# Kernel optimization log

Hardware: AMD Instinct MI355X
Metric: run time of the kernel (lower is better)

## Reference

```python
import jax, jax.numpy as jnp
import numpy as np

B, N_IN, N_VALUES = 1_000_000, 59, 12


def setup_inputs() -> dict:
    key = jax.random.key(0)
    k1, k2, k3, k4 = jax.random.split(key, 4)
    neural_activity = jax.random.normal(k1, (B, N_IN), dtype=jnp.float32)
    cards_by_trials = jax.random.randint(k2, (B, 4, 3), 0, N_VALUES, dtype=jnp.int64)
    # nn.Linear params: weight [out, in], bias [out]
    W = jax.random.normal(k3, (N_VALUES, N_IN), dtype=jnp.float32) / np.sqrt(N_IN)
    b = jax.random.normal(k4, (N_VALUES,), dtype=jnp.float32) * 0.01
    return {"neural_activity": neural_activity, "cards_by_trials": cards_by_trials, "W": W, "b": b}


def reference(neural_activity, cards_by_trials, W, b):
    # feature_values: [B, n_values]
    feature_values = jnp.einsum("bi,vi->bv", neural_activity, W) + b
    # fused gather + per-card sum (replaces the Python double loop)
    batch_idx = jnp.arange(feature_values.shape[0])[:, None, None]  # [B,1,1]
    gathered = feature_values[batch_idx, cards_by_trials]           # [B,4,3]
    card_values = jnp.sum(gathered, axis=-1)                        # [B,4]
    return card_values
```

## Files before the change

kernel.cpp:

```cpp
#include <hip/hip_runtime.h>

#define N_IN 59
#define N_VALUES 12
#define BLOCK 256
#define WROWS 16
#define TILE_F (WROWS * N_IN)
#define TILE_BYTES (TILE_F * 4)
#define TILE_STRIDE_F 952
#define FV_STRIDE 12
#define WL_STRIDE 68
#define WL_FLOATS (16 * WL_STRIDE)
#define GRID 3125
#define WAVES 4
#define TOTWAVES (GRID * WAVES)
#define TPW 5

typedef __attribute__((ext_vector_type(4))) float  f32x4;
typedef __attribute__((ext_vector_type(8))) __bf16 bf16x8;

#define STAGE(tt)                                                              \
    do {                                                                       \
        const char* _s = (const char*)act + (long)(tt) * TILE_BYTES + lane * 16;\
        char* _d = (char*)tw;                                                  \
        __builtin_amdgcn_global_load_lds(                                      \
            (const __attribute__((address_space(1))) void*)(_s),               \
            (__attribute__((address_space(3))) void*)(_d), 16, 0, 0);          \
        __builtin_amdgcn_global_load_lds(                                      \
            (const __attribute__((address_space(1))) void*)(_s + 1024),        \
            (__attribute__((address_space(3))) void*)(_d + 1024), 16, 0, 0);   \
        __builtin_amdgcn_global_load_lds(                                      \
            (const __attribute__((address_space(1))) void*)(_s + 2048),        \
            (__attribute__((address_space(3))) void*)(_d + 2048), 16, 0, 0);   \
        if (lane < 44) {                                                       \
            __builtin_amdgcn_global_load_lds(                                  \
                (const __attribute__((address_space(1))) void*)(_s + 3072),    \
                (__attribute__((address_space(3))) void*)(_d + 3072), 16, 0, 0);\
        }                                                                      \
    } while (0)

__global__ __launch_bounds__(BLOCK, 8) void value_model_kernel(
    const float* __restrict__ act,
    const int*   __restrict__ cards,
    const float* __restrict__ W,
    const float* __restrict__ bias,
    float* __restrict__ out)
{
    __shared__ float aLds[WAVES * TILE_STRIDE_F];
    __shared__ float xLds[WL_FLOATS];

    const int tid  = threadIdx.x;
    const int wave = tid >> 6;
    const int lane = tid & 63;
    float* tw = aLds + wave * TILE_STRIDE_F;

    for (int i = tid; i < WL_FLOATS; i += BLOCK) xLds[i] = 0.0f;
    if (lane < TILE_STRIDE_F - TILE_F) tw[TILE_F + lane] = 0.0f;
    asm volatile("s_waitcnt lgkmcnt(0)" ::: "memory");
    __builtin_amdgcn_s_barrier();

    for (int i = tid; i < N_VALUES * N_IN; i += BLOCK) {
        int v = i / N_IN;
        int j = i - v * N_IN;
        xLds[v * WL_STRIDE + j] = W[i];
    }
    asm volatile("s_waitcnt lgkmcnt(0)" ::: "memory");
    __builtin_amdgcn_s_barrier();

    const int colA = lane & 15, gA = lane >> 4;
    bf16x8 bf0, bf1;
    {
        const float* wp = xLds + colA * WL_STRIDE + gA * 8;
        #pragma unroll
        for (int e = 0; e < 8; ++e) bf0[e] = (__bf16)wp[e];
        #pragma unroll
        for (int e = 0; e < 8; ++e) bf1[e] = (__bf16)wp[32 + e];
    }
    float bv = 0.0f;
    if (colA < N_VALUES) bv = bias[colA];
    asm volatile("s_waitcnt lgkmcnt(0)" ::: "memory");
    __builtin_amdgcn_s_barrier();

    float* fw = xLds + wave * (WROWS * FV_STRIDE);
    const int r4 = lane >> 2, c4 = lane & 3;

    long t = (long)blockIdx.x * WAVES + wave;
    int ca, cb, cc;
    {
        const int* cp = cards + (t * WROWS + r4) * 12 + c4 * 3;
        ca = cp[0]; cb = cp[1]; cc = cp[2];
    }
    STAGE(t);

    #pragma unroll
    for (int it = 0; it < TPW; ++it) {
        asm volatile("s_waitcnt vmcnt(0) lgkmcnt(0)" ::: "memory");
        __builtin_amdgcn_wave_barrier();

        bf16x8 a0, a1;
        const float* p = tw + colA * N_IN + gA * 8;
        #pragma unroll
        for (int e = 0; e < 8; ++e) a0[e] = (__bf16)p[e];
        #pragma unroll
        for (int e = 0; e < 8; ++e) a1[e] = (__bf16)p[32 + e];

        f32x4 acc = {bv, bv, bv, bv};
        acc = __builtin_amdgcn_mfma_f32_16x16x32_bf16(a0, bf0, acc, 0, 0, 0);
        acc = __builtin_amdgcn_mfma_f32_16x16x32_bf16(a1, bf1, acc, 0, 0, 0);

        long tn = t + TOTWAVES;
        int na = 0, nb = 0, nc = 0;
        if (it + 1 < TPW) {
            STAGE(tn);
            const int* cp = cards + (tn * WROWS + r4) * 12 + c4 * 3;
            na = cp[0]; nb = cp[1]; nc = cp[2];
        }

        if (colA < N_VALUES) {
            #pragma unroll
            for (int j = 0; j < 4; ++j)
                fw[(gA * 4 + j) * FV_STRIDE + colA] = acc[j];
        }
        asm volatile("s_waitcnt lgkmcnt(0)" ::: "memory");
        __builtin_amdgcn_wave_barrier();

        const float* fv = fw + r4 * FV_STRIDE;
        long grow = t * WROWS + r4;
        out[grow * 4 + c4] = fv[ca] + fv[cb] + fv[cc];

        ca = na; cb = nb; cc = nc; t = tn;
    }
}

extern "C" void kernel_launch(void* const* d_in, const int* in_sizes, int n_in,
                              void* d_out, int out_size, void* d_ws, size_t ws_size,
                              hipStream_t stream) {
    const float* act   = (const float*)d_in[0];
    const int*   cards = (const int*)d_in[1];
    const float* W     = (const float*)d_in[2];
    const float* bias  = (const float*)d_in[3];
    float* out = (float*)d_out;

    value_model_kernel<<<GRID, BLOCK, 0, stream>>>(act, cards, W, bias, out);
}
```

Baseline: 50.60 us.

## Double-buffer activation tiles in a persistent grid-stride loop

Replaces the fixed five-tiles-per-wave schedule over 3125 blocks with a persistent grid of 1024 blocks that grid-strides over tiles. Each wave now has two LDS buffers, so the next tile's async global-to-LDS load and its card loads are issued before the current tile's MFMA and gather. A partial vmcnt wait lets the current tile be consumed while the next one is still in flight. The aim is to hide load latency and remove the tail wave of blocks, at the cost of more LDS per block and a lower launch-bound occupancy.

```diff
diff --git a/kernel.cpp b/kernel.cpp
--- a/kernel.cpp
+++ b/kernel.cpp
@@ -6,55 +6,59 @@
 #define WROWS 16
 #define TILE_F (WROWS * N_IN)
 #define TILE_BYTES (TILE_F * 4)
-#define TILE_STRIDE_F 952
+#define BUF_STRIDE_F 952
 #define FV_STRIDE 12
 #define WL_STRIDE 68
 #define WL_FLOATS (16 * WL_STRIDE)
-#define GRID 3125
+#define GRID 1024
 #define WAVES 4
-#define TOTWAVES (GRID * WAVES)
-#define TPW 5
+#define NWAVES (GRID * WAVES)
+#define NT 62500
 
 typedef __attribute__((ext_vector_type(4))) float  f32x4;
 typedef __attribute__((ext_vector_type(8))) __bf16 bf16x8;
 
-#define STAGE(tt)                                                              \
-    do {                                                                       \
-        const char* _s = (const char*)act + (long)(tt) * TILE_BYTES + lane * 16;\
-        char* _d = (char*)tw;                                                  \
-        __builtin_amdgcn_global_load_lds(                                      \
-            (const __attribute__((address_space(1))) void*)(_s),               \
-            (__attribute__((address_space(3))) void*)(_d), 16, 0, 0);          \
-        __builtin_amdgcn_global_load_lds(                                      \
-            (const __attribute__((address_space(1))) void*)(_s + 1024),        \
-            (__attribute__((address_space(3))) void*)(_d + 1024), 16, 0, 0);   \
-        __builtin_amdgcn_global_load_lds(                                      \
-            (const __attribute__((address_space(1))) void*)(_s + 2048),        \
-            (__attribute__((address_space(3))) void*)(_d + 2048), 16, 0, 0);   \
-        if (lane < 44) {                                                       \
-            __builtin_amdgcn_global_load_lds(                                  \
-                (const __attribute__((address_space(1))) void*)(_s + 3072),    \
-                (__attribute__((address_space(3))) void*)(_d + 3072), 16, 0, 0);\
-        }                                                                      \
-    } while (0)
+static __device__ __forceinline__ void stage_tile(const float* act, int tt,
+                                                  int lane, float* dst) {
+    const char* s = (const char*)act + (long)tt * TILE_BYTES + lane * 16;
+    char* d = (char*)dst;
+    __builtin_amdgcn_global_load_lds(
+        (const __attribute__((address_space(1))) void*)(s),
+        (__attribute__((address_space(3))) void*)(d), 16, 0, 0);
+    __builtin_amdgcn_global_load_lds(
+        (const __attribute__((address_space(1))) void*)(s + 1024),
+        (__attribute__((address_space(3))) void*)(d + 1024), 16, 0, 0);
+    __builtin_amdgcn_global_load_lds(
+        (const __attribute__((address_space(1))) void*)(s + 2048),
+        (__attribute__((address_space(3))) void*)(d + 2048), 16, 0, 0);
+    if (lane < 44) {
+        __builtin_amdgcn_global_load_lds(
+            (const __attribute__((address_space(1))) void*)(s + 3072),
+            (__attribute__((address_space(3))) void*)(d + 3072), 16, 0, 0);
+    }
+}
 
-__global__ __launch_bounds__(BLOCK, 8) void value_model_kernel(
+__global__ __launch_bounds__(BLOCK, 4) void value_model_kernel(
     const float* __restrict__ act,
     const int*   __restrict__ cards,
     const float* __restrict__ W,
     const float* __restrict__ bias,
     float* __restrict__ out)
 {
-    __shared__ float aLds[WAVES * TILE_STRIDE_F];
+    __shared__ float aLds[WAVES * 2 * BUF_STRIDE_F];
     __shared__ float xLds[WL_FLOATS];
 
     const int tid  = threadIdx.x;
     const int wave = tid >> 6;
     const int lane = tid & 63;
-    float* tw = aLds + wave * TILE_STRIDE_F;
+    float* buf0 = aLds + wave * (2 * BUF_STRIDE_F);
+    float* buf1 = buf0 + BUF_STRIDE_F;
 
     for (int i = tid; i < WL_FLOATS; i += BLOCK) xLds[i] = 0.0f;
-    if (lane < TILE_STRIDE_F - TILE_F) tw[TILE_F + lane] = 0.0f;
+    if (lane < BUF_STRIDE_F - TILE_F) {
+        buf0[TILE_F + lane] = 0.0f;
+        buf1[TILE_F + lane] = 0.0f;
+    }
     asm volatile("s_waitcnt lgkmcnt(0)" ::: "memory");
     __builtin_amdgcn_s_barrier();
 
@@ -83,21 +87,33 @@
     float* fw = xLds + wave * (WROWS * FV_STRIDE);
     const int r4 = lane >> 2, c4 = lane & 3;
 
-    long t = (long)blockIdx.x * WAVES + wave;
+    int t = blockIdx.x * WAVES + wave;
     int ca, cb, cc;
     {
-        const int* cp = cards + (t * WROWS + r4) * 12 + c4 * 3;
+        const int* cp = cards + ((long)t * WROWS + r4) * 12 + c4 * 3;
         ca = cp[0]; cb = cp[1]; cc = cp[2];
+        stage_tile(act, t, lane, buf0);
     }
-    STAGE(t);
+    int cur = 0;
+    while (t < NT) {
+        const int nxt = t + NWAVES;
+        const bool hasNext = nxt < NT;
 
-    #pragma unroll
-    for (int it = 0; it < TPW; ++it) {
-        asm volatile("s_waitcnt vmcnt(0) lgkmcnt(0)" ::: "memory");
+        int na = 0, nb = 0, nc2 = 0;
+        if (hasNext) {
+            const int* cp = cards + ((long)nxt * WROWS + r4) * 12 + c4 * 3;
+            na = cp[0]; nb = cp[1]; nc2 = cp[2];
+            stage_tile(act, nxt, lane, cur ? buf0 : buf1);
+        }
+
+        if (hasNext) asm volatile("s_waitcnt vmcnt(7)" ::: "memory");
+        else         asm volatile("s_waitcnt vmcnt(0)" ::: "memory");
+        __builtin_amdgcn_sched_barrier(0);
         __builtin_amdgcn_wave_barrier();
 
+        float* tw = cur ? buf1 : buf0;
+        const float* p = tw + colA * N_IN + gA * 8;
         bf16x8 a0, a1;
-        const float* p = tw + colA * N_IN + gA * 8;
         #pragma unroll
         for (int e = 0; e < 8; ++e) a0[e] = (__bf16)p[e];
         #pragma unroll
@@ -106,14 +122,6 @@
         f32x4 acc = {bv, bv, bv, bv};
         acc = __builtin_amdgcn_mfma_f32_16x16x32_bf16(a0, bf0, acc, 0, 0, 0);
         acc = __builtin_amdgcn_mfma_f32_16x16x32_bf16(a1, bf1, acc, 0, 0, 0);
-
-        long tn = t + TOTWAVES;
-        int na = 0, nb = 0, nc = 0;
-        if (it + 1 < TPW) {
-            STAGE(tn);
-            const int* cp = cards + (tn * WROWS + r4) * 12 + c4 * 3;
-            na = cp[0]; nb = cp[1]; nc = cp[2];
-        }
 
         if (colA < N_VALUES) {
             #pragma unroll
@@ -124,10 +132,11 @@
         __builtin_amdgcn_wave_barrier();
 
         const float* fv = fw + r4 * FV_STRIDE;
-        long grow = t * WROWS + r4;
-        out[grow * 4 + c4] = fv[ca] + fv[cb] + fv[cc];
+        out[((long)t * WROWS + r4) * 4 + c4] = fv[ca] + fv[cb] + fv[cc];
 
-        ca = na; cb = nb; cc = nc; t = tn;
+        ca = na; cb = nb; cc = nc2;
+        cur ^= 1;
+        t = nxt;
     }
 }
 
```

Measured after the change: 50.86 us. No clear change (+0.5%).
